# Kernel optimization log

Measured on AMD Instinct MI355X. Metric: run time of the kernel, lower is better.

Reference implementation:

```python
import jax, jax.numpy as jnp
import numpy as np


def _sample_plane(plane, coords):
    """torch.nn.functional.grid_sample, mode='bilinear', padding_mode='zeros',
    align_corners=True.  plane: [C,H,W]; coords: [N,2] with (x,y) in [-1,1]
    (x indexes W, y indexes H, as in torch grid convention).  Returns [N,C]."""
    C, H, W = plane.shape
    x = (coords[:, 0] + 1.0) * 0.5 * (W - 1)
    y = (coords[:, 1] + 1.0) * 0.5 * (H - 1)
    x0f = jnp.floor(x); y0f = jnp.floor(y)
    wx = x - x0f; wy = y - y0f

    def corner(yi, xi):
        valid = (xi >= 0) & (xi < W) & (yi >= 0) & (yi < H)
        xc = jnp.clip(xi, 0, W - 1).astype(jnp.int32)
        yc = jnp.clip(yi, 0, H - 1).astype(jnp.int32)
        return plane[:, yc, xc] * valid.astype(plane.dtype)  # [C,N]

    v00 = corner(y0f, x0f)
    v01 = corner(y0f, x0f + 1)
    v10 = corner(y0f + 1, x0f)
    v11 = corner(y0f + 1, x0f + 1)
    out = (v00 * (1 - wx) * (1 - wy) + v01 * wx * (1 - wy)
           + v10 * (1 - wx) * wy + v11 * wx * wy)
    return out.T  # [N,C]


_sample_batched = jax.vmap(_sample_plane)  # [B,C,H,W],[B,N,2] -> [B,N,C]


def setup_inputs() -> dict:
    key = jax.random.key(0)
    ks = jax.random.split(key, 8)
    B, N, C, R = 4, 131072, 32, 256
    triplanes = jax.random.normal(ks[0], (B, 3, C, R, R), jnp.float32) * 0.1
    coordinates = jax.random.uniform(ks[1], (B, N, 3), jnp.float32, -1.0, 1.0)
    # MLP weights ~ frequency_init(30) / first_layer_sine_init scales
    w0 = jax.random.uniform(ks[2], (128, C), jnp.float32, -1.0 / C, 1.0 / C)
    b0 = jnp.zeros((128,), jnp.float32)
    s1 = np.sqrt(6.0 / 128) / 30.0
    w1 = jax.random.uniform(ks[3], (128, 128), jnp.float32, -s1, s1)
    b1 = jnp.zeros((128,), jnp.float32)
    w2 = jax.random.uniform(ks[4], (1, 128), jnp.float32, -s1, s1)
    b2 = jnp.zeros((1,), jnp.float32)
    return {"triplanes": triplanes, "coordinates": coordinates,
            "w0": w0, "b0": b0, "w1": w1, "b1": b1, "w2": w2, "b2": b2}


def reference(triplanes, coordinates, w0, b0, w1, b1, w2, b2):
    # triplanes: [B,3,C,R,R]; coordinates: [B,N,3]
    xy = _sample_batched(triplanes[:, 0], coordinates[..., 0:2])   # (x,y)
    yz = _sample_batched(triplanes[:, 1], coordinates[..., 1:3])   # (y,z)
    xz = _sample_batched(triplanes[:, 2], coordinates[..., 0::2])  # (x,z)
    features = xy * yz * xz  # aggregate_fn == 'prod'; [B,N,C]
    h = jax.nn.relu(jnp.einsum('bnc,hc->bnh', features, w0) + b0)
    h = jax.nn.relu(jnp.einsum('bnh,gh->bng', h, w1) + b1)
    return jnp.einsum('bng,og->bno', h, w2) + b2  # [B,N,1]
```

## Files before the change

### kernel.cpp

```cpp
#include <hip/hip_runtime.h>
#include <hip/hip_bf16.h>
#include <cstddef>

#define RES 256
#define NCH 32
#define NPT 131072
#define NB  4

typedef _Float16 half8 __attribute__((ext_vector_type(8)));
typedef _Float16 half4 __attribute__((ext_vector_type(4)));
typedef float    f32x4 __attribute__((ext_vector_type(4)));

#define FEAT_STRIDE 40
#define H0_STRIDE   136
#define WAVE_LDS    (32 * H0_STRIDE)
#define WPB         4

__global__ __launch_bounds__(256) void transpose_prep_kernel(
    const float* __restrict__ in,
    const float* __restrict__ w0, const float* __restrict__ w1,
    _Float16* __restrict__ out,
    _Float16* __restrict__ w0h, _Float16* __restrict__ w1h)
{
    const int bp = blockIdx.y;
    const int t  = threadIdx.x;

    if (bp == 12) {
        const int i = blockIdx.x * 256 + t;
        if (i < 128 * NCH)  w0h[i] = (_Float16)(w0[i] * 16.0f);
        if (i < 128 * 128)  w1h[i] = (_Float16)w1[i];
        return;
    }

    __shared__ _Float16 tileh[NCH][RES + 8];
    const int y = blockIdx.x;

    const float4* src4 = (const float4*)(in + (size_t)bp * NCH * RES * RES);
    const int lane64 = t & 63;
    const int cq     = t >> 6;
    #pragma unroll
    for (int i = 0; i < 8; ++i) {
        const int c = cq * 8 + i;
        const float4 v = src4[(size_t)c * (RES * RES / 4) + y * (RES / 4) + lane64];
        half4 h = { (_Float16)v.x, (_Float16)v.y, (_Float16)v.z, (_Float16)v.w };
        *(half4*)&tileh[c][lane64 * 4] = h;
    }
    __syncthreads();

    _Float16* dst = out + ((size_t)bp * RES * RES + (size_t)y * RES) * NCH;
    const int x = t;
    #pragma unroll
    for (int cg = 0; cg < 4; ++cg) {
        half8 h;
        #pragma unroll
        for (int k = 0; k < 8; ++k)
            h[k] = tileh[cg * 8 + k][x];
        *(half8*)&dst[(size_t)x * NCH + cg * 8] = h;
    }
}

__global__ __launch_bounds__(256, 4) void fused_kernel(
    const _Float16* __restrict__ planesT,
    const float* __restrict__ coords,
    const _Float16* __restrict__ w0h,
    const _Float16* __restrict__ w1h,
    const float* __restrict__ b0, const float* __restrict__ b1,
    const float* __restrict__ w2, const float* __restrict__ b2,
    float* __restrict__ out)
{
    __shared__ __align__(16) _Float16 wbase_all[WPB * WAVE_LDS];

    const int wave = threadIdx.x >> 6;
    const int tid  = threadIdx.x & 63;
    _Float16* wbase = wbase_all + wave * WAVE_LDS;

    const int l15  = tid & 15;
    const int quad = tid >> 4;
    const int gchunk = blockIdx.x * WPB + wave;

    {
        const int p  = tid >> 1;
        const int hf = tid & 1;
        const int gp = gchunk * 32 + p;
        const int b  = gp >> 17;
        const float cx = coords[(size_t)gp * 3 + 0];
        const float cy = coords[(size_t)gp * 3 + 1];
        const float cz = coords[(size_t)gp * 3 + 2];

        int   offs[12];
        float wgt[12];
        #pragma unroll
        for (int pl = 0; pl < 3; ++pl) {
            const float u = (pl == 0) ? cx : (pl == 1) ? cy : cx;
            const float v = (pl == 0) ? cy : cz;

            const float fx = (u + 1.0f) * 0.5f * (RES - 1);
            const float fy = (v + 1.0f) * 0.5f * (RES - 1);
            const float x0f = floorf(fx), y0f = floorf(fy);
            const float wx = fx - x0f, wy = fy - y0f;
            const int x0 = (int)x0f, y0 = (int)y0f;
            const bool vx1 = (x0 + 1) < RES;
            const bool vy1 = (y0 + 1) < RES;
            const int x1 = vx1 ? x0 + 1 : RES - 1;
            const int y1 = vy1 ? y0 + 1 : RES - 1;

            float w00 = (1.0f - wx) * (1.0f - wy);
            float w01 = wx * (1.0f - wy);
            float w10 = (1.0f - wx) * wy;
            float w11 = wx * wy;
            if (!vx1) { w01 = 0.0f; w11 = 0.0f; }
            if (!vy1) { w10 = 0.0f; w11 = 0.0f; }

            const int pbase = ((b * 3 + pl) << 21) + (hf << 4);
            offs[pl * 4 + 0] = pbase + (y0 << 13) + (x0 << 5);
            offs[pl * 4 + 1] = pbase + (y0 << 13) + (x1 << 5);
            offs[pl * 4 + 2] = pbase + (y1 << 13) + (x0 << 5);
            offs[pl * 4 + 3] = pbase + (y1 << 13) + (x1 << 5);
            wgt[pl * 4 + 0] = w00; wgt[pl * 4 + 1] = w01;
            wgt[pl * 4 + 2] = w10; wgt[pl * 4 + 3] = w11;
        }

        half8 L0[12], L1[12];
        #pragma unroll
        for (int i = 0; i < 12; ++i) {
            const _Float16* cp = planesT + (size_t)(unsigned)offs[i];
            L0[i] = *(const half8*)cp;
            L1[i] = *(const half8*)(cp + 8);
        }

        float prod[16];
        #pragma unroll
        for (int pl = 0; pl < 3; ++pl) {
            #pragma unroll
            for (int k = 0; k < 8; ++k) {
                const float t0 =
                    fmaf((float)L0[pl*4+3][k], wgt[pl*4+3],
                    fmaf((float)L0[pl*4+2][k], wgt[pl*4+2],
                    fmaf((float)L0[pl*4+1][k], wgt[pl*4+1],
                         (float)L0[pl*4+0][k] * wgt[pl*4+0])));
                const float t1 =
                    fmaf((float)L1[pl*4+3][k], wgt[pl*4+3],
                    fmaf((float)L1[pl*4+2][k], wgt[pl*4+2],
                    fmaf((float)L1[pl*4+1][k], wgt[pl*4+1],
                         (float)L1[pl*4+0][k] * wgt[pl*4+0])));
                if (pl == 0) { prod[k] = t0;  prod[8 + k] = t1; }
                else         { prod[k] *= t0; prod[8 + k] *= t1; }
            }
        }

        half8 o0, o1;
        #pragma unroll
        for (int k = 0; k < 8; ++k) {
            o0[k] = (_Float16)(prod[k]     * 256.0f);
            o1[k] = (_Float16)(prod[8 + k] * 256.0f);
        }
        *(half8*)&wbase[p * FEAT_STRIDE + hf * 16 + 0] = o0;
        *(half8*)&wbase[p * FEAT_STRIDE + hf * 16 + 8] = o1;
    }

    half8 a0[2];
    #pragma unroll
    for (int mt = 0; mt < 2; ++mt)
        a0[mt] = *(const half8*)&wbase[(mt * 16 + l15) * FEAT_STRIDE + quad * 8];

    float b0v[8], b1v[8], w2s[8];
    #pragma unroll
    for (int nt = 0; nt < 8; ++nt) {
        b0v[nt] = b0[nt * 16 + l15] * 4096.0f;
        b1v[nt] = b1[nt * 16 + l15] * 4096.0f;
        w2s[nt] = w2[nt * 16 + l15] * (1.0f / 4096.0f);
    }

    #pragma unroll 1
    for (int nt = 0; nt < 8; ++nt) {
        const half8 bfr = *(const half8*)&w0h[(nt * 16 + l15) * NCH + quad * 8];
        f32x4 acc[2];
        #pragma unroll
        for (int mt = 0; mt < 2; ++mt) {
            acc[mt] = (f32x4){0.f, 0.f, 0.f, 0.f};
            acc[mt] = __builtin_amdgcn_mfma_f32_16x16x32_f16(
                a0[mt], bfr, acc[mt], 0, 0, 0);
        }
        #pragma unroll
        for (int mt = 0; mt < 2; ++mt)
            #pragma unroll
            for (int r = 0; r < 4; ++r) {
                const float hval = fmaxf(acc[mt][r] + b0v[nt], 0.0f);
                wbase[(mt * 16 + quad * 4 + r) * H0_STRIDE + nt * 16 + l15]
                    = (_Float16)hval;
            }
    }

    half8 a1[2][4];
    #pragma unroll
    for (int mt = 0; mt < 2; ++mt)
        #pragma unroll
        for (int ks = 0; ks < 4; ++ks)
            a1[mt][ks] = *(const half8*)
                &wbase[(mt * 16 + l15) * H0_STRIDE + ks * 32 + quad * 8];

    float part[2][4];
    #pragma unroll
    for (int mt = 0; mt < 2; ++mt)
        #pragma unroll
        for (int r = 0; r < 4; ++r) part[mt][r] = 0.0f;

    #pragma unroll 2
    for (int nt = 0; nt < 8; ++nt) {
        f32x4 acc[2];
        #pragma unroll
        for (int mt = 0; mt < 2; ++mt) acc[mt] = (f32x4){0.f, 0.f, 0.f, 0.f};
        #pragma unroll
        for (int ks = 0; ks < 4; ++ks) {
            const half8 bfr = *(const half8*)
                &w1h[(nt * 16 + l15) * 128 + ks * 32 + quad * 8];
            #pragma unroll
            for (int mt = 0; mt < 2; ++mt)
                acc[mt] = __builtin_amdgcn_mfma_f32_16x16x32_f16(
                    a1[mt][ks], bfr, acc[mt], 0, 0, 0);
        }
        #pragma unroll
        for (int mt = 0; mt < 2; ++mt)
            #pragma unroll
            for (int r = 0; r < 4; ++r)
                part[mt][r] = fmaf(w2s[nt], fmaxf(acc[mt][r] + b1v[nt], 0.0f),
                                   part[mt][r]);
    }

    #pragma unroll
    for (int mt = 0; mt < 2; ++mt)
        #pragma unroll
        for (int r = 0; r < 4; ++r) {
            float s = part[mt][r];
            s += __shfl_xor(s, 1);
            s += __shfl_xor(s, 2);
            s += __shfl_xor(s, 4);
            s += __shfl_xor(s, 8);
            part[mt][r] = s;
        }

    if (l15 == 0) {
        const float bias2 = b2[0];
        const int base = gchunk * 32;
        #pragma unroll
        for (int mt = 0; mt < 2; ++mt)
            #pragma unroll
            for (int r = 0; r < 4; ++r)
                out[base + mt * 16 + quad * 4 + r] = part[mt][r] + bias2;
    }
}

__global__ __launch_bounds__(256) void fused_fallback(
    const float* __restrict__ planes, const float* __restrict__ coords,
    const float* __restrict__ w0, const float* __restrict__ b0,
    const float* __restrict__ w1, const float* __restrict__ b1,
    const float* __restrict__ w2, const float* __restrict__ b2,
    float* __restrict__ out)
{
    const int t = blockIdx.x * 256 + threadIdx.x;
    const int b = t >> 17;
    const float cx = coords[(size_t)t * 3 + 0];
    const float cy = coords[(size_t)t * 3 + 1];
    const float cz = coords[(size_t)t * 3 + 2];
    float feat[NCH];
    #pragma unroll
    for (int p = 0; p < 3; ++p) {
        const float u = (p == 0) ? cx : (p == 1) ? cy : cx;
        const float v = (p == 0) ? cy : cz;
        const float fx = (u + 1.0f) * 0.5f * (RES - 1);
        const float fy = (v + 1.0f) * 0.5f * (RES - 1);
        const float x0f = floorf(fx), y0f = floorf(fy);
        const float wx = fx - x0f, wy = fy - y0f;
        const int x0 = (int)x0f, y0 = (int)y0f;
        const bool vx1 = (x0 + 1) < RES, vy1 = (y0 + 1) < RES;
        const int x1 = vx1 ? x0 + 1 : RES - 1;
        const int y1 = vy1 ? y0 + 1 : RES - 1;
        float w00 = (1.0f - wx) * (1.0f - wy), w01 = wx * (1.0f - wy);
        float w10 = (1.0f - wx) * wy, w11 = wx * wy;
        if (!vx1) { w01 = 0.0f; w11 = 0.0f; }
        if (!vy1) { w10 = 0.0f; w11 = 0.0f; }
        const float* base = planes + (size_t)(b * 3 + p) * NCH * RES * RES;
        const float* p00 = base + (size_t)y0 * RES + x0;
        const float* p01 = base + (size_t)y0 * RES + x1;
        const float* p10 = base + (size_t)y1 * RES + x0;
        const float* p11 = base + (size_t)y1 * RES + x1;
        #pragma unroll
        for (int c = 0; c < NCH; ++c) {
            const size_t off = (size_t)c * RES * RES;
            float s = p00[off] * w00;
            s = fmaf(p01[off], w01, s);
            s = fmaf(p10[off], w10, s);
            s = fmaf(p11[off], w11, s);
            if (p == 0) feat[c] = s; else feat[c] *= s;
        }
    }
    float h0[128];
    #pragma unroll
    for (int g = 0; g < 128; ++g) {
        const float* wr = w0 + g * NCH;
        float aA = b0[g], aB = 0.0f;
        #pragma unroll
        for (int c = 0; c < NCH; c += 2) {
            aA = fmaf(wr[c], feat[c], aA);
            aB = fmaf(wr[c + 1], feat[c + 1], aB);
        }
        h0[g] = fmaxf(aA + aB, 0.0f);
    }
    float o = b2[0];
    for (int g = 0; g < 128; ++g) {
        const float* wr = w1 + g * 128;
        float aA = b1[g], aB = 0.0f, aC = 0.0f, aD = 0.0f;
        #pragma unroll
        for (int h = 0; h < 128; h += 4) {
            aA = fmaf(wr[h], h0[h], aA);
            aB = fmaf(wr[h + 1], h0[h + 1], aB);
            aC = fmaf(wr[h + 2], h0[h + 2], aC);
            aD = fmaf(wr[h + 3], h0[h + 3], aD);
        }
        o = fmaf(fmaxf((aA + aB) + (aC + aD), 0.0f), w2[g], o);
    }
    out[t] = o;
}

extern "C" void kernel_launch(void* const* d_in, const int* in_sizes, int n_in,
                              void* d_out, int out_size, void* d_ws, size_t ws_size,
                              hipStream_t stream)
{
    const float* trip   = (const float*)d_in[0];
    const float* coords = (const float*)d_in[1];
    const float* w0     = (const float*)d_in[2];
    const float* b0     = (const float*)d_in[3];
    const float* w1     = (const float*)d_in[4];
    const float* b1     = (const float*)d_in[5];
    const float* w2     = (const float*)d_in[6];
    const float* b2     = (const float*)d_in[7];
    float* out = (float*)d_out;

    const size_t planesTBytes = (size_t)NB * 3 * RES * RES * NCH * 2;
    const size_t w0hBytes = 128 * NCH * 2;
    const size_t w1hBytes = 128 * 128 * 2;
    const size_t needed = planesTBytes + w0hBytes + w1hBytes;

    if (ws_size >= needed) {
        _Float16* planesT = (_Float16*)d_ws;
        _Float16* w0h     = (_Float16*)((char*)d_ws + planesTBytes);
        _Float16* w1h     = (_Float16*)((char*)d_ws + planesTBytes + w0hBytes);

        transpose_prep_kernel<<<dim3(RES, NB * 3 + 1), 256, 0, stream>>>(
            trip, w0, w1, planesT, w0h, w1h);
        fused_kernel<<<(NB * NPT) / (32 * WPB), 256, 0, stream>>>(
            planesT, coords, w0h, w1h, b0, b1, w2, b2, out);
    } else {
        fused_fallback<<<(NB * NPT) / 256, 256, 0, stream>>>(
            trip, coords, w0, b0, w1, b1, w2, b2, out);
    }
}
```

Baseline: 287.4 us.

## Sort sample points by Morton-ordered spatial cell before triplane gathering

Adds a counting sort (zero, histogram, scan, scatter kernels) that buckets points into 16^3 Morton-ordered cells per batch and writes permuted float4 coordinates plus a permutation index. The fused kernel then processes spatially nearby points together, so its bilinear gathers from the fp16 transposed planes should hit cache more often, and it scatters outputs back through the permutation. This costs four extra launches, atomics on coordinates, extra workspace, and a scattered output write. The old direct path is kept as a fallback for when workspace is too small.

After: 349.6 us. 1.22x slower.

```diff
diff --git a/kernel.cpp b/kernel.cpp
--- a/kernel.cpp
+++ b/kernel.cpp
@@ -15,6 +15,82 @@
 #define H0_STRIDE   136
 #define WAVE_LDS    (32 * H0_STRIDE)
 #define WPB         4
+
+#define NCELL_P_B   4096
+#define NCELL       (NB * NCELL_P_B)
+
+
+__device__ __forceinline__ int point_cell(float cx, float cy, float cz, int b)
+{
+    int ix = (int)floorf((cx + 1.0f) * 8.0f);
+    int iy = (int)floorf((cy + 1.0f) * 8.0f);
+    int iz = (int)floorf((cz + 1.0f) * 8.0f);
+    ix = ix < 0 ? 0 : (ix > 15 ? 15 : ix);
+    iy = iy < 0 ? 0 : (iy > 15 ? 15 : iy);
+    iz = iz < 0 ? 0 : (iz > 15 ? 15 : iz);
+    int m = 0;
+    #pragma unroll
+    for (int i = 0; i < 4; ++i) {
+        m |= ((ix >> i) & 1) << (3 * i + 0);
+        m |= ((iy >> i) & 1) << (3 * i + 1);
+        m |= ((iz >> i) & 1) << (3 * i + 2);
+    }
+    return (b << 12) | m;
+}
+
+__global__ __launch_bounds__(256) void zero_kernel(int* __restrict__ cnt)
+{
+    cnt[blockIdx.x * 256 + threadIdx.x] = 0;
+}
+
+__global__ __launch_bounds__(256) void hist_kernel(
+    const float* __restrict__ coords, int* __restrict__ cnt)
+{
+    const int pid = blockIdx.x * 256 + threadIdx.x;
+    const int b   = pid >> 17;
+    const float cx = coords[(size_t)pid * 3 + 0];
+    const float cy = coords[(size_t)pid * 3 + 1];
+    const float cz = coords[(size_t)pid * 3 + 2];
+    atomicAdd(&cnt[point_cell(cx, cy, cz, b)], 1);
+}
+
+__global__ __launch_bounds__(256) void scan_kernel(
+    const int* __restrict__ cnt, int* __restrict__ cursor)
+{
+    __shared__ int seg[256];
+    const int t = threadIdx.x;
+    int s = 0;
+    #pragma unroll 4
+    for (int i = 0; i < 64; ++i) s += cnt[t * 64 + i];
+    seg[t] = s;
+    __syncthreads();
+    for (int d = 1; d < 256; d <<= 1) {
+        int v = (t >= d) ? seg[t - d] : 0;
+        __syncthreads();
+        seg[t] += v;
+        __syncthreads();
+    }
+    int run = (t == 0) ? 0 : seg[t - 1];
+    for (int i = 0; i < 64; ++i) {
+        cursor[t * 64 + i] = run;
+        run += cnt[t * 64 + i];
+    }
+}
+
+__global__ __launch_bounds__(256) void scatter_kernel(
+    const float* __restrict__ coords, int* __restrict__ cursor,
+    int* __restrict__ perm, float* __restrict__ coords4)
+{
+    const int pid = blockIdx.x * 256 + threadIdx.x;
+    const int b   = pid >> 17;
+    const float cx = coords[(size_t)pid * 3 + 0];
+    const float cy = coords[(size_t)pid * 3 + 1];
+    const float cz = coords[(size_t)pid * 3 + 2];
+    const int pos = atomicAdd(&cursor[point_cell(cx, cy, cz, b)], 1);
+    perm[pos] = pid;
+    float4 v = make_float4(cx, cy, cz, __int_as_float(pid));
+    ((float4*)coords4)[pos] = v;
+}
 
 __global__ __launch_bounds__(256) void transpose_prep_kernel(
     const float* __restrict__ in,
@@ -59,9 +135,12 @@
     }
 }
 
-__global__ __launch_bounds__(256, 4) void fused_kernel(
+__global__ __attribute__((amdgcn_flat_work_group_size(256, 256)))
+__attribute__((amdgpu_waves_per_eu(4, 4)))
+void fused_kernel(
     const _Float16* __restrict__ planesT,
-    const float* __restrict__ coords,
+    const float* __restrict__ coords4,
+    const int* __restrict__ perm,
     const _Float16* __restrict__ w0h,
     const _Float16* __restrict__ w1h,
     const float* __restrict__ b0, const float* __restrict__ b1,
@@ -81,11 +160,10 @@
     {
         const int p  = tid >> 1;
         const int hf = tid & 1;
-        const int gp = gchunk * 32 + p;
-        const int b  = gp >> 17;
-        const float cx = coords[(size_t)gp * 3 + 0];
-        const float cy = coords[(size_t)gp * 3 + 1];
-        const float cz = coords[(size_t)gp * 3 + 2];
+        const float4 c4 = ((const float4*)coords4)[gchunk * 32 + p];
+        const float cx = c4.x, cy = c4.y, cz = c4.z;
+        const int pid = __float_as_int(c4.w);
+        const int b   = pid >> 17;
 
         int   offs[12];
         float wgt[12];
@@ -111,6 +189,196 @@
             if (!vx1) { w01 = 0.0f; w11 = 0.0f; }
             if (!vy1) { w10 = 0.0f; w11 = 0.0f; }
 
+            const int pbase = ((b * 3 + pl) << 21) + (hf << 4);
+            offs[pl * 4 + 0] = pbase + (y0 << 13) + (x0 << 5);
+            offs[pl * 4 + 1] = pbase + (y0 << 13) + (x1 << 5);
+            offs[pl * 4 + 2] = pbase + (y1 << 13) + (x0 << 5);
+            offs[pl * 4 + 3] = pbase + (y1 << 13) + (x1 << 5);
+            wgt[pl * 4 + 0] = w00; wgt[pl * 4 + 1] = w01;
+            wgt[pl * 4 + 2] = w10; wgt[pl * 4 + 3] = w11;
+        }
+
+        half8 L0[12], L1[12];
+        #pragma unroll
+        for (int i = 0; i < 12; ++i) {
+            const _Float16* cp = planesT + (size_t)(unsigned)offs[i];
+            L0[i] = *(const half8*)cp;
+            L1[i] = *(const half8*)(cp + 8);
+        }
+
+        float prod[16];
+        #pragma unroll
+        for (int pl = 0; pl < 3; ++pl) {
+            #pragma unroll
+            for (int k = 0; k < 8; ++k) {
+                const float t0 =
+                    fmaf((float)L0[pl*4+3][k], wgt[pl*4+3],
+                    fmaf((float)L0[pl*4+2][k], wgt[pl*4+2],
+                    fmaf((float)L0[pl*4+1][k], wgt[pl*4+1],
+                         (float)L0[pl*4+0][k] * wgt[pl*4+0])));
+                const float t1 =
+                    fmaf((float)L1[pl*4+3][k], wgt[pl*4+3],
+                    fmaf((float)L1[pl*4+2][k], wgt[pl*4+2],
+                    fmaf((float)L1[pl*4+1][k], wgt[pl*4+1],
+                         (float)L1[pl*4+0][k] * wgt[pl*4+0])));
+                if (pl == 0) { prod[k] = t0;  prod[8 + k] = t1; }
+                else         { prod[k] *= t0; prod[8 + k] *= t1; }
+            }
+        }
+
+        half8 o0, o1;
+        #pragma unroll
+        for (int k = 0; k < 8; ++k) {
+            o0[k] = (_Float16)(prod[k]     * 256.0f);
+            o1[k] = (_Float16)(prod[8 + k] * 256.0f);
+        }
+        *(half8*)&wbase[p * FEAT_STRIDE + hf * 16 + 0] = o0;
+        *(half8*)&wbase[p * FEAT_STRIDE + hf * 16 + 8] = o1;
+    }
+
+    half8 a0[2];
+    #pragma unroll
+    for (int mt = 0; mt < 2; ++mt)
+        a0[mt] = *(const half8*)&wbase[(mt * 16 + l15) * FEAT_STRIDE + quad * 8];
+
+    float b0v[8], b1v[8], w2s[8];
+    #pragma unroll
+    for (int nt = 0; nt < 8; ++nt) {
+        b0v[nt] = b0[nt * 16 + l15] * 4096.0f;
+        b1v[nt] = b1[nt * 16 + l15] * 4096.0f;
+        w2s[nt] = w2[nt * 16 + l15] * (1.0f / 4096.0f);
+    }
+
+    #pragma unroll 1
+    for (int nt = 0; nt < 8; ++nt) {
+        const half8 bfr = *(const half8*)&w0h[(nt * 16 + l15) * NCH + quad * 8];
+        f32x4 acc[2];
+        #pragma unroll
+        for (int mt = 0; mt < 2; ++mt) {
+            acc[mt] = (f32x4){0.f, 0.f, 0.f, 0.f};
+            acc[mt] = __builtin_amdgcn_mfma_f32_16x16x32_f16(
+                a0[mt], bfr, acc[mt], 0, 0, 0);
+        }
+        #pragma unroll
+        for (int mt = 0; mt < 2; ++mt)
+            #pragma unroll
+            for (int r = 0; r < 4; ++r) {
+                const float hval = fmaxf(acc[mt][r] + b0v[nt], 0.0f);
+                wbase[(mt * 16 + quad * 4 + r) * H0_STRIDE + nt * 16 + l15]
+                    = (_Float16)hval;
+            }
+    }
+
+    half8 a1[2][4];
+    #pragma unroll
+    for (int mt = 0; mt < 2; ++mt)
+        #pragma unroll
+        for (int ks = 0; ks < 4; ++ks)
+            a1[mt][ks] = *(const half8*)
+                &wbase[(mt * 16 + l15) * H0_STRIDE + ks * 32 + quad * 8];
+
+    float part[2][4];
+    #pragma unroll
+    for (int mt = 0; mt < 2; ++mt)
+        #pragma unroll
+        for (int r = 0; r < 4; ++r) part[mt][r] = 0.0f;
+
+    #pragma unroll 2
+    for (int nt = 0; nt < 8; ++nt) {
+        f32x4 acc[2];
+        #pragma unroll
+        for (int mt = 0; mt < 2; ++mt) acc[mt] = (f32x4){0.f, 0.f, 0.f, 0.f};
+        #pragma unroll
+        for (int ks = 0; ks < 4; ++ks) {
+            const half8 bfr = *(const half8*)
+                &w1h[(nt * 16 + l15) * 128 + ks * 32 + quad * 8];
+            #pragma unroll
+            for (int mt = 0; mt < 2; ++mt)
+                acc[mt] = __builtin_amdgcn_mfma_f32_16x16x32_f16(
+                    a1[mt][ks], bfr, acc[mt], 0, 0, 0);
+        }
+        #pragma unroll
+        for (int mt = 0; mt < 2; ++mt)
+            #pragma unroll
+            for (int r = 0; r < 4; ++r)
+                part[mt][r] = fmaf(w2s[nt], fmaxf(acc[mt][r] + b1v[nt], 0.0f),
+                                   part[mt][r]);
+    }
+
+    #pragma unroll
+    for (int mt = 0; mt < 2; ++mt)
+        #pragma unroll
+        for (int r = 0; r < 4; ++r) {
+            float s = part[mt][r];
+            s += __shfl_xor(s, 1);
+            s += __shfl_xor(s, 2);
+            s += __shfl_xor(s, 4);
+            s += __shfl_xor(s, 8);
+            part[mt][r] = s;
+        }
+
+    if (l15 == 0) {
+        const float bias2 = b2[0];
+        const int base = gchunk * 32;
+        #pragma unroll
+        for (int mt = 0; mt < 2; ++mt)
+            #pragma unroll
+            for (int r = 0; r < 4; ++r)
+                out[perm[base + mt * 16 + quad * 4 + r]] = part[mt][r] + bias2;
+    }
+}
+
+__global__ __attribute__((amdgcn_flat_work_group_size(256, 256)))
+__attribute__((amdgpu_waves_per_eu(4, 4)))
+void fused_kernel_direct(
+    const _Float16* __restrict__ planesT,
+    const float* __restrict__ coords,
+    const _Float16* __restrict__ w0h,
+    const _Float16* __restrict__ w1h,
+    const float* __restrict__ b0, const float* __restrict__ b1,
+    const float* __restrict__ w2, const float* __restrict__ b2,
+    float* __restrict__ out)
+{
+    __shared__ __align__(16) _Float16 wbase_all[WPB * WAVE_LDS];
+
+    const int wave = threadIdx.x >> 6;
+    const int tid  = threadIdx.x & 63;
+    _Float16* wbase = wbase_all + wave * WAVE_LDS;
+
+    const int l15  = tid & 15;
+    const int quad = tid >> 4;
+    const int gchunk = blockIdx.x * WPB + wave;
+
+    {
+        const int p  = tid >> 1;
+        const int hf = tid & 1;
+        const int gp = gchunk * 32 + p;
+        const int b  = gp >> 17;
+        const float cx = coords[(size_t)gp * 3 + 0];
+        const float cy = coords[(size_t)gp * 3 + 1];
+        const float cz = coords[(size_t)gp * 3 + 2];
+
+        int   offs[12];
+        float wgt[12];
+        #pragma unroll
+        for (int pl = 0; pl < 3; ++pl) {
+            const float u = (pl == 0) ? cx : (pl == 1) ? cy : cx;
+            const float v = (pl == 0) ? cy : cz;
+            const float fx = (u + 1.0f) * 0.5f * (RES - 1);
+            const float fy = (v + 1.0f) * 0.5f * (RES - 1);
+            const float x0f = floorf(fx), y0f = floorf(fy);
+            const float wx = fx - x0f, wy = fy - y0f;
+            const int x0 = (int)x0f, y0 = (int)y0f;
+            const bool vx1 = (x0 + 1) < RES;
+            const bool vy1 = (y0 + 1) < RES;
+            const int x1 = vx1 ? x0 + 1 : RES - 1;
+            const int y1 = vy1 ? y0 + 1 : RES - 1;
+            float w00 = (1.0f - wx) * (1.0f - wy);
+            float w01 = wx * (1.0f - wy);
+            float w10 = (1.0f - wx) * wy;
+            float w11 = wx * wy;
+            if (!vx1) { w01 = 0.0f; w11 = 0.0f; }
+            if (!vy1) { w10 = 0.0f; w11 = 0.0f; }
             const int pbase = ((b * 3 + pl) << 21) + (hf << 4);
             offs[pl * 4 + 0] = pbase + (y0 << 13) + (x0 << 5);
             offs[pl * 4 + 1] = pbase + (y0 << 13) + (x1 << 5);
@@ -337,18 +605,40 @@
     float* out = (float*)d_out;
 
     const size_t planesTBytes = (size_t)NB * 3 * RES * RES * NCH * 2;
-    const size_t w0hBytes = 128 * NCH * 2;
-    const size_t w1hBytes = 128 * 128 * 2;
-    const size_t needed = planesTBytes + w0hBytes + w1hBytes;
-
-    if (ws_size >= needed) {
+    const size_t w0hBytes  = 128 * NCH * 2;
+    const size_t w1hBytes  = 128 * 128 * 2;
+    const size_t permBytes = (size_t)NB * NPT * 4;
+    const size_t cntBytes  = (size_t)NCELL * 4;
+    const size_t c4Bytes   = (size_t)NB * NPT * 16;
+    const size_t needed  = planesTBytes + w0hBytes + w1hBytes;
+    const size_t needed2 = needed + permBytes + 2 * cntBytes + c4Bytes;
+
+    if (ws_size >= needed2) {
+        char* ws = (char*)d_ws;
+        _Float16* planesT = (_Float16*)ws;
+        _Float16* w0h     = (_Float16*)(ws + planesTBytes);
+        _Float16* w1h     = (_Float16*)(ws + planesTBytes + w0hBytes);
+        int*   perm    = (int*)(ws + needed);
+        int*   cnt     = (int*)(ws + needed + permBytes);
+        int*   cursor  = (int*)(ws + needed + permBytes + cntBytes);
+        float* coords4 = (float*)(ws + needed + permBytes + 2 * cntBytes);
+
+        zero_kernel<<<NCELL / 256, 256, 0, stream>>>(cnt);
+        hist_kernel<<<(NB * NPT) / 256, 256, 0, stream>>>(coords, cnt);
+        scan_kernel<<<1, 256, 0, stream>>>(cnt, cursor);
+        scatter_kernel<<<(NB * NPT) / 256, 256, 0, stream>>>(
+            coords, cursor, perm, coords4);
+        transpose_prep_kernel<<<dim3(RES, NB * 3 + 1), 256, 0, stream>>>(
+            trip, w0, w1, planesT, w0h, w1h);
+        fused_kernel<<<(NB * NPT) / (32 * WPB), 256, 0, stream>>>(
+            planesT, coords4, perm, w0h, w1h, b0, b1, w2, b2, out);
+    } else if (ws_size >= needed) {
         _Float16* planesT = (_Float16*)d_ws;
         _Float16* w0h     = (_Float16*)((char*)d_ws + planesTBytes);
         _Float16* w1h     = (_Float16*)((char*)d_ws + planesTBytes + w0hBytes);
-
         transpose_prep_kernel<<<dim3(RES, NB * 3 + 1), 256, 0, stream>>>(
             trip, w0, w1, planesT, w0h, w1h);
-        fused_kernel<<<(NB * NPT) / (32 * WPB), 256, 0, stream>>>(
+        fused_kernel_direct<<<(NB * NPT) / (32 * WPB), 256, 0, stream>>>(
             planesT, coords, w0h, w1h, b0, b1, w2, b2, out);
     } else {
         fused_fallback<<<(NB * NPT) / 256, 256, 0, stream>>>(
```
